# Kernel tuning notes

Measured on AMD Instinct MI355X. Metric: run time of the kernel, lower is better.

The kernel has to match this reference:

```python
import jax, jax.numpy as jnp
import numpy as np

N_SRC = 100000
N_DST = 100000
E = 1600000
IN_DIM = 128
OUT_DIM = 64
NEG_SLOPE = 0.01  # torch F.leaky_relu default


def setup_inputs() -> dict:
    key = jax.random.key(0)
    ks = jax.random.split(key, 7)
    g = np.sqrt(2.0)  # relu gain used in xavier init; scale only, not exactness-critical
    return {
        "h_src": jax.random.normal(ks[0], (N_SRC, IN_DIM), jnp.float32),
        "h_dst": jax.random.normal(ks[1], (N_DST, IN_DIM), jnp.float32),
        "src_idx": jax.random.randint(ks[2], (E,), 0, N_SRC, jnp.int32),
        "dst_idx": jax.random.randint(ks[3], (E,), 0, N_DST, jnp.int32),
        "W_src": (jax.random.normal(ks[4], (OUT_DIM, IN_DIM), jnp.float32) * (g / np.sqrt(IN_DIM))),
        "W_dst": (jax.random.normal(ks[5], (OUT_DIM, IN_DIM), jnp.float32) * (g / np.sqrt(IN_DIM))),
        "attn_w": (jax.random.normal(ks[6], (1, 2 * OUT_DIM), jnp.float32) * (g / np.sqrt(2 * OUT_DIM))),
        "item_user": 0,
    }


def reference(h_src, h_dst, src_idx, dst_idx, W_src, W_dst, attn_w, item_user):
    # node projections (fc_src / fc_dst, no bias)
    z_src = h_src @ W_src.T                      # [N_src, OUT]
    if item_user:
        z_src = jax.nn.softplus(z_src)
    z_dst = h_dst @ W_dst.T                      # [N_dst, OUT]

    # attn_fc(cat(z_src_e, z_dst_e)) == z_src @ a_l + z_dst @ a_r (precompute per node)
    a_l = attn_w[0, :OUT_DIM]
    a_r = attn_w[0, OUT_DIM:]
    el = z_src @ a_l                             # [N_src]
    er = z_dst @ a_r                             # [N_dst]

    e = jax.nn.leaky_relu(el[src_idx] + er[dst_idx], NEG_SLOPE)  # [E]

    # segment softmax over edges grouped by dst (stable: subtract per-dst max)
    m = jax.ops.segment_max(e, dst_idx, num_segments=N_DST)      # [N_dst], -inf for empty
    ex = jnp.exp(e - m[dst_idx])                                  # [E]
    denom = jax.ops.segment_sum(ex, dst_idx, num_segments=N_DST)  # [N_dst]
    alpha = ex / denom[dst_idx]                                   # [E]

    # weighted scatter-sum of source messages; empty dst nodes get zeros (DGL default)
    msgs = alpha[:, None] * z_src[src_idx]                        # [E, OUT]
    h_out = jax.ops.segment_sum(msgs, dst_idx, num_segments=N_DST)  # [N_dst, OUT]
    return h_out
```

## Files before the change

### kernel.cpp

```cpp
#include <hip/hip_runtime.h>
#include <math.h>

#define NSRC 100000
#define NDST 100000
#define NE   1600000
#define IND  128
#define OUTD 64
#define SLOPE 0.01f
#define CAP  48
#define CSTR 16

#define FILL_BLOCKS 782
#define ER_BLOCKS   782
#define ZTILES      1563
#define P1_BLOCKS (FILL_BLOCKS + ER_BLOCKS + ZTILES)

typedef _Float16       f16x8 __attribute__((ext_vector_type(8)));
typedef float          f32x4 __attribute__((ext_vector_type(4)));
typedef unsigned short u16x8 __attribute__((ext_vector_type(8)));

__device__ __forceinline__ float softplus_f(float x) {
    return (x > 20.f) ? x : log1pf(__expf(x));
}
__device__ __forceinline__ unsigned short f2bf(float f) {
    unsigned u = __float_as_uint(f);
    return (unsigned short)((u + 0x7FFFu + ((u >> 16) & 1u)) >> 16);
}
__device__ __forceinline__ float bf2f(unsigned short h) {
    return __uint_as_float(((unsigned)h) << 16);
}

__device__ __forceinline__ void zsrc_body(float* vsrc, int tile,
                                          const float* __restrict__ h_src,
                                          const float* __restrict__ W_src,
                                          const float* __restrict__ attn_w,
                                          int iu,
                                          unsigned short* __restrict__ z16,
                                          float* __restrict__ el) {
    const int t = threadIdx.x;
    if (t < IND) {
        float a = 0.f;
#pragma unroll 8
        for (int o = 0; o < OUTD; ++o)
            a = fmaf(W_src[o * IND + t], attn_w[o], a);
        vsrc[t] = a;
    }
    __syncthreads();

    const int w = t >> 6, l = t & 63;
    const int r = l & 15, q = l >> 4;
    const int rowA  = tile * 64 + w * 16 + r;
    const int rowAc = (rowA < NSRC) ? rowA : (NSRC - 1);

    f32x4 acc[4];
#pragma unroll
    for (int c = 0; c < 4; ++c) acc[c] = (f32x4)0.f;
    float elp = 0.f;

#pragma unroll
    for (int ks = 0; ks < 4; ++ks) {
        const float* ap = h_src + rowAc * IND + ks * 32 + q * 8;
        float4 a0 = *(const float4*)ap;
        float4 a1 = *(const float4*)(ap + 4);
        const float* vp = vsrc + ks * 32 + q * 8;
        float4 v0 = *(const float4*)vp;
        float4 v1 = *(const float4*)(vp + 4);
        elp = fmaf(a0.x, v0.x, elp); elp = fmaf(a0.y, v0.y, elp);
        elp = fmaf(a0.z, v0.z, elp); elp = fmaf(a0.w, v0.w, elp);
        elp = fmaf(a1.x, v1.x, elp); elp = fmaf(a1.y, v1.y, elp);
        elp = fmaf(a1.z, v1.z, elp); elp = fmaf(a1.w, v1.w, elp);
        f16x8 af;
        af[0] = (_Float16)a0.x; af[1] = (_Float16)a0.y;
        af[2] = (_Float16)a0.z; af[3] = (_Float16)a0.w;
        af[4] = (_Float16)a1.x; af[5] = (_Float16)a1.y;
        af[6] = (_Float16)a1.z; af[7] = (_Float16)a1.w;
#pragma unroll
        for (int c = 0; c < 4; ++c) {
            const float* bp = W_src + (16 * c + r) * IND + ks * 32 + q * 8;
            float4 b0 = *(const float4*)bp;
            float4 b1 = *(const float4*)(bp + 4);
            f16x8 bf;
            bf[0] = (_Float16)b0.x; bf[1] = (_Float16)b0.y;
            bf[2] = (_Float16)b0.z; bf[3] = (_Float16)b0.w;
            bf[4] = (_Float16)b1.x; bf[5] = (_Float16)b1.y;
            bf[6] = (_Float16)b1.z; bf[7] = (_Float16)b1.w;
            acc[c] = __builtin_amdgcn_mfma_f32_16x16x32_f16(af, bf, acc[c], 0, 0, 0);
        }
    }

    if (!iu) {
        elp += __shfl_xor(elp, 16);
        elp += __shfl_xor(elp, 32);
        if (q == 0 && rowA < NSRC) el[rowA] = elp;
    } else {
#pragma unroll
        for (int c = 0; c < 4; ++c)
#pragma unroll
            for (int j = 0; j < 4; ++j) acc[c][j] = softplus_f(acc[c][j]);
        float ac0 = attn_w[r], ac1 = attn_w[16 + r], ac2 = attn_w[32 + r], ac3 = attn_w[48 + r];
#pragma unroll
        for (int j = 0; j < 4; ++j) {
            float s = fmaf(acc[0][j], ac0, fmaf(acc[1][j], ac1,
                      fmaf(acc[2][j], ac2, acc[3][j] * ac3)));
            s += __shfl_xor(s, 1); s += __shfl_xor(s, 2);
            s += __shfl_xor(s, 4); s += __shfl_xor(s, 8);
            const int row = tile * 64 + w * 16 + q * 4 + j;
            if (r == 0 && row < NSRC) el[row] = s;
        }
    }

    const int rowD0 = tile * 64 + w * 16 + q * 4;
#pragma unroll
    for (int j = 0; j < 4; ++j) {
        const int row = rowD0 + j;
        if (row < NSRC) {
#pragma unroll
            for (int c = 0; c < 4; ++c)
                z16[row * OUTD + 16 * c + r] = f2bf(acc[c][j]);
        }
    }
}

__device__ __forceinline__ void er_body(float* v, int eb,
                                        const float* __restrict__ h_dst,
                                        const float* __restrict__ W_dst,
                                        const float* __restrict__ attn_w,
                                        float* __restrict__ er) {
    const int t = threadIdx.x;
    if (t < IND) {
        float a = 0.f;
#pragma unroll 8
        for (int o = 0; o < OUTD; ++o)
            a = fmaf(W_dst[o * IND + t], attn_w[OUTD + o], a);
        v[t] = a;
    }
    __syncthreads();
    const int wv = t >> 6, l = t & 63, hh = l >> 5, c = l & 31;
    float4 vv = *(const float4*)(v + c * 4);
    const int row0 = eb * 128;
#pragma unroll 4
    for (int p = 0; p < 16; ++p) {
        int row = row0 + p * 8 + wv * 2 + hh;
        if (row < NDST) {
            float4 x = *(const float4*)(h_dst + row * IND + c * 4);
            float s = fmaf(x.x, vv.x, fmaf(x.y, vv.y, fmaf(x.z, vv.z, x.w * vv.w)));
            s += __shfl_xor(s, 16); s += __shfl_xor(s, 8);
            s += __shfl_xor(s, 4);  s += __shfl_xor(s, 2);
            s += __shfl_xor(s, 1);
            if (c == 0) er[row] = s;
        }
    }
}

__device__ __forceinline__ void fill_body(int fb, const int* __restrict__ src,
                                          const int* __restrict__ dst,
                                          int* __restrict__ cnt,
                                          int* __restrict__ slot) {
    int j = fb * 2048 + threadIdx.x;
#pragma unroll 2
    for (int it = 0; it < 8; ++it, j += 256) {
        if (j < NE) {
            int d = dst[j];
            int s = src[j];
            int p = atomicAdd(&cnt[d * CSTR], 1);
            if (p < CAP) slot[d * CAP + p] = s;
        }
    }
}

__global__ __launch_bounds__(256) void k_p1(
        const float* __restrict__ h_src, const float* __restrict__ W_src,
        const float* __restrict__ attn_w, const int* __restrict__ item_user,
        const float* __restrict__ h_dst, const float* __restrict__ W_dst,
        const int* __restrict__ src_idx, const int* __restrict__ dst_idx,
        unsigned short* __restrict__ z16, float* __restrict__ el,
        float* __restrict__ er, int* __restrict__ cnt,
        int* __restrict__ slot) {
    __shared__ float smem[IND];
    const int b = blockIdx.x;
    if (b < FILL_BLOCKS) {
        fill_body(b, src_idx, dst_idx, cnt, slot);
    } else if (b < FILL_BLOCKS + ER_BLOCKS) {
        er_body(smem, b - FILL_BLOCKS, h_dst, W_dst, attn_w, er);
    } else {
        zsrc_body(smem, b - FILL_BLOCKS - ER_BLOCKS, h_src, W_src, attn_w,
                  *item_user, z16, el);
    }
}

__global__ __launch_bounds__(256) void k_aggregate(
        const int* __restrict__ cnt, const int* __restrict__ slot,
        const float* __restrict__ el, const float* __restrict__ er,
        const unsigned short* __restrict__ z16, float* __restrict__ out) {
    const int wave = threadIdx.x >> 6, lane = threadIdx.x & 63;
    const int d = blockIdx.x * 4 + wave;
    const int degRaw = cnt[d * CSTR];
    const float er_d = er[d];
    int s = 0;
    if (lane < CAP) s = slot[d * CAP + lane];
    s = ((unsigned)s < (unsigned)NSRC) ? s : 0;

    const int deg = (degRaw < 0) ? 0 : ((degRaw > CAP) ? CAP : degRaw);
    float ex = 0.f;
    if (lane < deg) {
        float e = el[s] + er_d;
        e = (e > 0.f) ? e : SLOPE * e;
        ex = __expf(e);
    }
    float dsum = ex;
#pragma unroll
    for (int off = 1; off < 64; off <<= 1) dsum += __shfl_xor(dsum, off);

    const int g = lane >> 3, gl = lane & 7;
    float acc[8];
#pragma unroll
    for (int k = 0; k < 8; ++k) acc[k] = 0.f;
    for (int base = 0; base < deg; base += 8) {
        const int i = base + g;
        const int   si  = __shfl(s, i);
        const float exi = __shfl(ex, i);
        if (i < deg) {
            u16x8 zz = *(const u16x8*)(z16 + si * OUTD + gl * 8);
#pragma unroll
            for (int k = 0; k < 8; ++k) acc[k] = fmaf(exi, bf2f(zz[k]), acc[k]);
        }
    }
#pragma unroll
    for (int off = 8; off <= 32; off <<= 1) {
#pragma unroll
        for (int k = 0; k < 8; ++k) acc[k] += __shfl_xor(acc[k], off);
    }
    if (g == 0) {
        float inv = (deg > 0 && dsum > 0.f) ? 1.f / dsum : 0.f;
        float4 o0 = float4{acc[0] * inv, acc[1] * inv, acc[2] * inv, acc[3] * inv};
        float4 o1 = float4{acc[4] * inv, acc[5] * inv, acc[6] * inv, acc[7] * inv};
        *(float4*)(out + d * OUTD + gl * 8)     = o0;
        *(float4*)(out + d * OUTD + gl * 8 + 4) = o1;
    }
}

extern "C" void kernel_launch(void* const* d_in, const int* in_sizes, int n_in,
                              void* d_out, int out_size, void* d_ws, size_t ws_size,
                              hipStream_t stream) {
    const float* h_src   = (const float*)d_in[0];
    const float* h_dst   = (const float*)d_in[1];
    const int*   src_idx = (const int*)d_in[2];
    const int*   dst_idx = (const int*)d_in[3];
    const float* W_src   = (const float*)d_in[4];
    const float* W_dst   = (const float*)d_in[5];
    const float* attn_w  = (const float*)d_in[6];
    const int*   item_u  = (const int*)d_in[7];
    float* out = (float*)d_out;

    char* ws = (char*)d_ws;
    unsigned short* z16 = (unsigned short*)(ws);
    float* el   = (float*)(ws + 12800000);
    float* er   = (float*)(ws + 13200000);
    int*   cnt  = (int*)  (ws + 13600000);
    int*   slot = (int*)  (ws + 20000000);

    hipMemsetAsync(cnt, 0, NDST * CSTR * 4, stream);

    k_p1       <<<P1_BLOCKS, 256, 0, stream>>>(h_src, W_src, attn_w, item_u,
                                               h_dst, W_dst, src_idx, dst_idx,
                                               z16, el, er, cnt, slot);
    k_aggregate<<<25000,     256, 0, stream>>>(cnt, slot, el, er, z16, out);
}
```

Baseline: 305.8 us.

## Make aggregate kernel persistent with per-wave destination chunks and prefetching

The aggregate kernel now launches a fixed grid of 2048 blocks. Each wave processes a contiguous chunk of about 13 destination nodes instead of one node per wave. Degrees and er values for the chunk are loaded once per lane. The next node's slot indices and el values are prefetched while the current node is accumulated, to hide gather latency and cut launch/scheduling overhead. The trade-off is fewer waves in flight for latency hiding, plus a leftover dead code block.

```diff
diff --git a/kernel.cpp b/kernel.cpp
--- a/kernel.cpp
+++ b/kernel.cpp
@@ -14,6 +14,10 @@
 #define ER_BLOCKS   782
 #define ZTILES      1563
 #define P1_BLOCKS (FILL_BLOCKS + ER_BLOCKS + ZTILES)
+
+#define AGG_BLOCKS 2048
+#define AGG_WAVES (AGG_BLOCKS * 4)
+#define CHUNK ((NDST + AGG_WAVES - 1) / AGG_WAVES)
 
 typedef _Float16       f16x8 __attribute__((ext_vector_type(8)));
 typedef float          f32x4 __attribute__((ext_vector_type(4)));
@@ -192,50 +196,84 @@
         const int* __restrict__ cnt, const int* __restrict__ slot,
         const float* __restrict__ el, const float* __restrict__ er,
         const unsigned short* __restrict__ z16, float* __restrict__ out) {
-    const int wave = threadIdx.x >> 6, lane = threadIdx.x & 63;
-    const int d = blockIdx.x * 4 + wave;
-    const int degRaw = cnt[d * CSTR];
-    const float er_d = er[d];
+    const int wid  = blockIdx.x * 4 + (threadIdx.x >> 6);
+    const int lane = threadIdx.x & 63;
+    const int d0 = wid * CHUNK;
+    if (d0 >= NDST) return;
+    const int n = min(NDST - d0, CHUNK);
+
+    int   cnL = 0;
+    float erL = 0.f;
+    if (lane < n) {
+        cnL = cnt[(d0 + lane) * CSTR];
+        erL = er[d0 + lane];
+    }
+
     int s = 0;
-    if (lane < CAP) s = slot[d * CAP + lane];
+    if (lane < CAP) s = slot[d0 * CAP + lane];
     s = ((unsigned)s < (unsigned)NSRC) ? s : 0;
-
-    const int deg = (degRaw < 0) ? 0 : ((degRaw > CAP) ? CAP : degRaw);
-    float ex = 0.f;
-    if (lane < deg) {
-        float e = el[s] + er_d;
-        e = (e > 0.f) ? e : SLOPE * e;
-        ex = __expf(e);
-    }
-    float dsum = ex;
-#pragma unroll
-    for (int off = 1; off < 64; off <<= 1) dsum += __shfl_xor(dsum, off);
+    {
+        int deg0 = __shfl(cnL, 0);
+        deg0 = (deg0 < 0) ? 0 : ((deg0 > CAP) ? CAP : deg0);
+    }
+    int   degC = __shfl(cnL, 0);
+    degC = (degC < 0) ? 0 : ((degC > CAP) ? CAP : degC);
+    float elv = (lane < degC) ? el[s] : 0.f;
 
     const int g = lane >> 3, gl = lane & 7;
-    float acc[8];
-#pragma unroll
-    for (int k = 0; k < 8; ++k) acc[k] = 0.f;
-    for (int base = 0; base < deg; base += 8) {
-        const int i = base + g;
-        const int   si  = __shfl(s, i);
-        const float exi = __shfl(ex, i);
-        if (i < deg) {
-            u16x8 zz = *(const u16x8*)(z16 + si * OUTD + gl * 8);
-#pragma unroll
-            for (int k = 0; k < 8; ++k) acc[k] = fmaf(exi, bf2f(zz[k]), acc[k]);
-        }
-    }
-#pragma unroll
-    for (int off = 8; off <= 32; off <<= 1) {
-#pragma unroll
-        for (int k = 0; k < 8; ++k) acc[k] += __shfl_xor(acc[k], off);
-    }
-    if (g == 0) {
-        float inv = (deg > 0 && dsum > 0.f) ? 1.f / dsum : 0.f;
-        float4 o0 = float4{acc[0] * inv, acc[1] * inv, acc[2] * inv, acc[3] * inv};
-        float4 o1 = float4{acc[4] * inv, acc[5] * inv, acc[6] * inv, acc[7] * inv};
-        *(float4*)(out + d * OUTD + gl * 8)     = o0;
-        *(float4*)(out + d * OUTD + gl * 8 + 4) = o1;
+
+    for (int i = 0; i < n; ++i) {
+        const int d = d0 + i;
+
+        int sN = 0;
+        if (i + 1 < n) {
+            if (lane < CAP) sN = slot[(d + 1) * CAP + lane];
+        }
+
+        const float er_d = __shfl(erL, i);
+        float ex = 0.f;
+        if (lane < degC) {
+            float e = elv + er_d;
+            e = (e > 0.f) ? e : SLOPE * e;
+            ex = __expf(e);
+        }
+        float dsum = ex;
+#pragma unroll
+        for (int off = 1; off < 64; off <<= 1) dsum += __shfl_xor(dsum, off);
+
+        float acc[8];
+#pragma unroll
+        for (int k = 0; k < 8; ++k) acc[k] = 0.f;
+        for (int base = 0; base < degC; base += 8) {
+            const int i2 = base + g;
+            const int   si  = __shfl(s, i2);
+            const float exi = __shfl(ex, i2);
+            if (i2 < degC) {
+                u16x8 zz = *(const u16x8*)(z16 + si * OUTD + gl * 8);
+#pragma unroll
+                for (int k = 0; k < 8; ++k) acc[k] = fmaf(exi, bf2f(zz[k]), acc[k]);
+            }
+        }
+#pragma unroll
+        for (int off = 8; off <= 32; off <<= 1) {
+#pragma unroll
+            for (int k = 0; k < 8; ++k) acc[k] += __shfl_xor(acc[k], off);
+        }
+        if (g == 0) {
+            float inv = (degC > 0 && dsum > 0.f) ? 1.f / dsum : 0.f;
+            float4 o0 = float4{acc[0] * inv, acc[1] * inv, acc[2] * inv, acc[3] * inv};
+            float4 o1 = float4{acc[4] * inv, acc[5] * inv, acc[6] * inv, acc[7] * inv};
+            *(float4*)(out + d * OUTD + gl * 8)     = o0;
+            *(float4*)(out + d * OUTD + gl * 8 + 4) = o1;
+        }
+
+        if (i + 1 < n) {
+            int degN = __shfl(cnL, i + 1);
+            degN = (degN < 0) ? 0 : ((degN > CAP) ? CAP : degN);
+            sN = ((unsigned)sN < (unsigned)NSRC) ? sN : 0;
+            float elN = (lane < degN) ? el[sN] : 0.f;
+            s = sN; elv = elN; degC = degN;
+        }
     }
 }
 
@@ -261,8 +299,8 @@
 
     hipMemsetAsync(cnt, 0, NDST * CSTR * 4, stream);
 
-    k_p1       <<<P1_BLOCKS, 256, 0, stream>>>(h_src, W_src, attn_w, item_u,
-                                               h_dst, W_dst, src_idx, dst_idx,
-                                               z16, el, er, cnt, slot);
-    k_aggregate<<<25000,     256, 0, stream>>>(cnt, slot, el, er, z16, out);
-}
+    k_p1       <<<P1_BLOCKS,  256, 0, stream>>>(h_src, W_src, attn_w, item_u,
+                                                h_dst, W_dst, src_idx, dst_idx,
+                                                z16, el, er, cnt, slot);
+    k_aggregate<<<AGG_BLOCKS, 256, 0, stream>>>(cnt, slot, el, er, z16, out);
+}
```

Result: no change. 306.2 us (+0.1%).
